# Optimization experiments

Hardware: AMD Instinct MI355X
Metric: run time of the kernel (lower is better)

## Reference

```python
import jax, jax.numpy as jnp
import numpy as np
from jax import lax

# QuantumDMRGLayer (isolated_labelnode=True) as a pure MPS chain contraction.
# Per sample: contract each site's (2,m[,m]) tensor with the 2-dim input vector
# over the physical leg, then multiply the resulting bond matrices along the
# chain, inserting the (m,m,nblabels) output tensor after site pos_label.

B, L, M, NBL = 2048, 196, 16, 10  # batch, dimvec, bond_len, nblabels


def setup_inputs() -> dict:
    key = jax.random.key(0)
    k_in, k_mid, k_l, k_r, k_out = jax.random.split(key, 5)
    # std chosen for numerical stability of a 196-long matrix product:
    # each site matrix is x0*A[0]+x1*A[1] with x~N(0,1), so effective per-site
    # gain ~ std*sqrt(2*m); std = 1/sqrt(2*m) keeps the product O(1).
    std = 1.0 / np.sqrt(2.0 * M)
    inputs = jax.random.normal(k_in, (B, L, 2), dtype=jnp.float32)
    eye2m = jnp.eye(M, dtype=jnp.float32)[:2, :]  # eye(max(2,m))[0:2,:] -> (2, m)
    A_left = eye2m + 1e-3 * jax.random.normal(k_l, (2, M), dtype=jnp.float32)
    A_right = eye2m + 1e-3 * jax.random.normal(k_r, (2, M), dtype=jnp.float32)
    A_mid = std * jax.random.normal(k_mid, (L - 2, 2, M, M), dtype=jnp.float32)
    T_out = (1.0 / np.sqrt(M)) * jax.random.normal(k_out, (M, M, NBL), dtype=jnp.float32)
    return {
        "inputs": inputs,
        "A_left": A_left,
        "A_mid": A_mid,
        "A_right": A_right,
        "T_out": T_out,
        "pos_label": 98,
    }


def reference(inputs, A_left, A_mid, A_right, T_out, pos_label):
    # Contract physical legs: interior site i (1..L-2) -> batched (m,m) matrix.
    mats = jnp.einsum("bsd,sdij->sbij", inputs[:, 1:-1, :], A_mid)  # (L-2, B, m, m)
    v_left = jnp.einsum("bd,dm->bm", inputs[:, 0, :], A_left)       # (B, m)
    v_right = jnp.einsum("bd,dm->bm", inputs[:, -1, :], A_right)    # (B, m)

    def step_l(v, Mx):  # v @ M, batched
        return jnp.einsum("bm,bmn->bn", v, Mx), None

    def step_r(v, Mx):  # M @ v, batched (sweep from the right end inward)
        return jnp.einsum("bmn,bn->bm", Mx, v), None

    # sites 1..pos_label feed the left bond of the output node,
    # sites pos_label+1..L-2 feed the right bond.
    left, _ = lax.scan(step_l, v_left, mats[:pos_label])
    right, _ = lax.scan(step_r, v_right, mats[pos_label:], reverse=True)
    return jnp.einsum("bm,mnl,bn->bl", left, T_out, right)  # (B, nblabels)
```

## Files before the change

### kernel.cpp

```cpp
#include <hip/hip_runtime.h>


typedef __attribute__((ext_vector_type(8))) short short8;
typedef __attribute__((ext_vector_type(16))) float floatx16;

#define GSITE_DW 512
#define GDIR_DW (100 * GSITE_DW)
#define STATE_DW (2 * GDIR_DW)

__device__ __forceinline__ unsigned bf16_rne(unsigned u) {
    return (u + 0x7FFFu + ((u >> 16) & 1u)) >> 16;
}

__global__ __launch_bounds__(256)
void prep_kernel(const float* __restrict__ AM, unsigned* __restrict__ WS)
{
    int t = blockIdx.x * 256 + threadIdx.x;
    const int w    = t & 3;  t >>= 2;
    const int lane = t & 63; t >>= 6;
    const int p    = t % 100;
    const int dir  = t / 100;
    const int kb = (lane >> 5) << 3;
    const int r  = lane & 31;
    const int rr = (r & 0x13) | ((r & 4) << 1) | ((r & 8) >> 1);
    const int d = rr >> 4, nn = rr & 15;
    const int lim = dir ? 96 : 98;
    const int a = dir ? (193 - p) : p;
    const int k0 = kb + 2 * w;
    float g0 = 0.f, g1 = 0.f;
    if (p < lim) {
        const float* Ab = AM + a * 512 + d * 256;
        if (dir == 0) { g0 = Ab[k0 * 16 + nn]; g1 = Ab[(k0 + 1) * 16 + nn]; }
        else          { g0 = Ab[nn * 16 + k0]; g1 = Ab[nn * 16 + k0 + 1]; }
    }
    const unsigned u0 = __float_as_uint(g0), u1 = __float_as_uint(g1);
    const unsigned h0 = bf16_rne(u0), h1 = bf16_rne(u1);
    const float l0f = g0 - __uint_as_float(h0 << 16);
    const float l1f = g1 - __uint_as_float(h1 << 16);
    const unsigned lo0 = bf16_rne(__float_as_uint(l0f));
    const unsigned lo1 = bf16_rne(__float_as_uint(l1f));
    unsigned* gp = WS + (dir * 100 + p) * GSITE_DW;
    gp[lane * 4 + w]       = (h1 << 16) | h0;
    gp[256 + lane * 4 + w] = (lo1 << 16) | lo0;
}

__global__ __launch_bounds__(64, 1)
void chain_kernel(const float* __restrict__ X,
                  const float* __restrict__ AL,
                  const float* __restrict__ AR,
                  const unsigned* __restrict__ WS,
                  float* __restrict__ WST)
{
    const int lane = threadIdx.x;
    const int dir  = blockIdx.x & 1;
    const int s    = (blockIdx.x >> 1) * 32 + (lane & 31);
    const int kb   = (lane >> 5) << 3;
    const float* Xs = X + s * 392;
    const unsigned* Gb = WS + dir * GDIR_DW + lane * 4;
    const int lim = dir ? 96 : 98;

    float w[8];
    int4 vh4, vl4;
    auto pack = [&]() {
#pragma unroll
        for (int q = 0; q < 4; ++q) {
            const unsigned u0 = __float_as_uint(w[2 * q]);
            const unsigned u1 = __float_as_uint(w[2 * q + 1]);
            const unsigned h0 = u0 & 0xFFFF0000u, h1 = u1 & 0xFFFF0000u;
            const float l0 = w[2 * q]     - __uint_as_float(h0);
            const float l1 = w[2 * q + 1] - __uint_as_float(h1);
            ((unsigned*)&vh4)[q] = h1 | (h0 >> 16);
            ((unsigned*)&vl4)[q] = (__float_as_uint(l1) & 0xFFFF0000u) |
                                   (__float_as_uint(l0) >> 16);
        }
    };

    const float* Ai = dir ? AR : AL;
    const float2 xi = *(const float2*)(Xs + (dir ? 390 : 0));
#pragma unroll
    for (int j = 0; j < 8; ++j)
        w[j] = xi.x * Ai[kb + j] + xi.y * Ai[16 + kb + j];
    pack();

    int4 GH[4], GL[4];
    float2 xr[4];
#pragma unroll
    for (int i = 0; i < 4; ++i) {
        GH[i] = *(const int4*)(Gb + i * GSITE_DW);
        GL[i] = *(const int4*)(Gb + i * GSITE_DW + 256);
        xr[i] = *(const float2*)(Xs + (dir ? (388 - 2 * i) : (2 + 2 * i)));
    }

    for (int c = 0; c < 25; ++c) {
#pragma unroll
        for (int j4 = 0; j4 < 4; ++j4) {
            const int p = 4 * c + j4;
            if (p < lim) {
                const short8 ah = *(short8*)&GH[j4];
                const short8 al = *(short8*)&GL[j4];
                const short8 bh = *(short8*)&vh4;
                const short8 bl = *(short8*)&vl4;
                floatx16 D = {};
                D = __builtin_amdgcn_mfma_f32_32x32x16_bf16(ah, bh, D, 0, 0, 0);
                D = __builtin_amdgcn_mfma_f32_32x32x16_bf16(ah, bl, D, 0, 0, 0);
                D = __builtin_amdgcn_mfma_f32_32x32x16_bf16(al, bh, D, 0, 0, 0);
                const float2 xs = xr[j4];
#pragma unroll
                for (int j = 0; j < 8; ++j)
                    w[j] = fmaf(xs.x, D[j], xs.y * D[j + 8]);
                pack();
            }
            const int pn = (p + 4 < 100) ? p + 4 : 99;
            GH[j4] = *(const int4*)(Gb + pn * GSITE_DW);
            GL[j4] = *(const int4*)(Gb + pn * GSITE_DW + 256);
            xr[j4] = *(const float2*)(Xs + (dir ? (388 - 2 * pn) : (2 + 2 * pn)));
        }
    }

    float* st = WST + (dir * 2048 + s) * 16 + kb;
    *(float4*)(st)     = make_float4(w[0], w[1], w[2], w[3]);
    *(float4*)(st + 4) = make_float4(w[4], w[5], w[6], w[7]);
}

__global__ __launch_bounds__(256)
void out_kernel(const float* __restrict__ T, const float* __restrict__ WST,
                float* __restrict__ OUT)
{
    __shared__ float sT[2560];
    const int tid = threadIdx.x;
    for (int k = tid; k < 640; k += 256)
        ((float4*)sT)[k] = ((const float4*)T)[k];
    __syncthreads();
    const int t = blockIdx.x * 256 + tid;
    const int s = t / 10, l = t - s * 10;
    const float* L = WST + s * 16;
    const float* R = WST + 2048 * 16 + s * 16;
    const float4 Ra = *(const float4*)(R);
    const float4 Rb = *(const float4*)(R + 4);
    const float4 Rc = *(const float4*)(R + 8);
    const float4 Rd = *(const float4*)(R + 12);
    float acc = 0.f;
#pragma unroll
    for (int m = 0; m < 16; ++m) {
        const float lm = L[m];
        const float* Tp = sT + m * 160 + l;
        acc = fmaf(lm * Ra.x, Tp[0],   acc);
        acc = fmaf(lm * Ra.y, Tp[10],  acc);
        acc = fmaf(lm * Ra.z, Tp[20],  acc);
        acc = fmaf(lm * Ra.w, Tp[30],  acc);
        acc = fmaf(lm * Rb.x, Tp[40],  acc);
        acc = fmaf(lm * Rb.y, Tp[50],  acc);
        acc = fmaf(lm * Rb.z, Tp[60],  acc);
        acc = fmaf(lm * Rb.w, Tp[70],  acc);
        acc = fmaf(lm * Rc.x, Tp[80],  acc);
        acc = fmaf(lm * Rc.y, Tp[90],  acc);
        acc = fmaf(lm * Rc.z, Tp[100], acc);
        acc = fmaf(lm * Rc.w, Tp[110], acc);
        acc = fmaf(lm * Rd.x, Tp[120], acc);
        acc = fmaf(lm * Rd.y, Tp[130], acc);
        acc = fmaf(lm * Rd.z, Tp[140], acc);
        acc = fmaf(lm * Rd.w, Tp[150], acc);
    }
    OUT[t] = acc;
}

extern "C" void kernel_launch(void* const* d_in, const int* in_sizes, int n_in,
                              void* d_out, int out_size, void* d_ws, size_t ws_size,
                              hipStream_t stream)
{
    const float* X  = (const float*)d_in[0];
    const float* AL = (const float*)d_in[1];
    const float* AM = (const float*)d_in[2];
    const float* AR = (const float*)d_in[3];
    const float* T  = (const float*)d_in[4];
    (void)in_sizes; (void)n_in; (void)out_size; (void)ws_size;
    unsigned* WS = (unsigned*)d_ws;
    float* WST   = (float*)d_ws + STATE_DW;
    float* OUT   = (float*)d_out;

    hipLaunchKernelGGL(prep_kernel,  dim3(200), dim3(256), 0, stream, AM, WS);
    hipLaunchKernelGGL(chain_kernel, dim3(128), dim3(64),  0, stream,
                       X, AL, AR, WS, WST);
    hipLaunchKernelGGL(out_kernel,   dim3(80),  dim3(256), 0, stream,
                       T, WST, OUT);
}
```

Before: 86.87 us.

## Split MPS chain into parallel segment matrix products, combine in output kernel

Replaces the serial 98/96-step vector-matrix chain per sample with 8 independent segments of about 24 sites each. Each segment computes a full 16x16 product matrix by starting from the identity, and the segments run as 8192 wavefronts instead of 128. The combine kernel applies the boundary vectors and then the four segment matrices per side, followed by the output-tensor contraction. This trades a much longer serial latency chain for more parallel work and extra memory traffic, since each segment writes a full matrix per sample.

```diff
diff --git a/kernel.cpp b/kernel.cpp
--- a/kernel.cpp
+++ b/kernel.cpp
@@ -6,7 +6,7 @@
 
 #define GSITE_DW 512
 #define GDIR_DW (100 * GSITE_DW)
-#define STATE_DW (2 * GDIR_DW)
+#define SEG_OFF_DW (2 * GDIR_DW)
 
 __device__ __forceinline__ unsigned bf16_rne(unsigned u) {
     return (u + 0x7FFFu + ((u >> 16) & 1u)) >> 16;
@@ -44,20 +44,27 @@
     gp[256 + lane * 4 + w] = (lo1 << 16) | lo0;
 }
 
-__global__ __launch_bounds__(64, 1)
-void chain_kernel(const float* __restrict__ X,
-                  const float* __restrict__ AL,
-                  const float* __restrict__ AR,
-                  const unsigned* __restrict__ WS,
-                  float* __restrict__ WST)
-{
-    const int lane = threadIdx.x;
-    const int dir  = blockIdx.x & 1;
-    const int s    = (blockIdx.x >> 1) * 32 + (lane & 31);
-    const int kb   = (lane >> 5) << 3;
+__global__ __launch_bounds__(256, 4)
+void seg_kernel(const float* __restrict__ X,
+                const unsigned* __restrict__ WS,
+                float* __restrict__ S)
+{
+    const int lane = threadIdx.x & 63;
+    const int gw   = blockIdx.x * 4 + (threadIdx.x >> 6);
+    const int seg  = gw >> 10;
+    const int pair = gw & 1023;
+    const int dir  = seg >> 2;
+    const int si   = seg & 3;
+    int p0, p1;
+    if (dir == 0) { p0 = (si < 2) ? 25 * si : 50 + 24 * (si - 2);
+                    p1 = p0 + ((si < 2) ? 25 : 24); }
+    else          { p0 = 24 * si; p1 = p0 + 24; }
+
+    const int m  = lane & 15;
+    const int s  = pair * 2 + ((lane >> 4) & 1);
+    const int kb = (lane >> 5) << 3;
     const float* Xs = X + s * 392;
     const unsigned* Gb = WS + dir * GDIR_DW + lane * 4;
-    const int lim = dir ? 96 : 98;
 
     float w[8];
     int4 vh4, vl4;
@@ -75,27 +82,26 @@
         }
     };
 
-    const float* Ai = dir ? AR : AL;
-    const float2 xi = *(const float2*)(Xs + (dir ? 390 : 0));
 #pragma unroll
     for (int j = 0; j < 8; ++j)
-        w[j] = xi.x * Ai[kb + j] + xi.y * Ai[16 + kb + j];
+        w[j] = (kb + j == m) ? 1.0f : 0.0f;
     pack();
 
     int4 GH[4], GL[4];
     float2 xr[4];
 #pragma unroll
     for (int i = 0; i < 4; ++i) {
-        GH[i] = *(const int4*)(Gb + i * GSITE_DW);
-        GL[i] = *(const int4*)(Gb + i * GSITE_DW + 256);
-        xr[i] = *(const float2*)(Xs + (dir ? (388 - 2 * i) : (2 + 2 * i)));
-    }
-
-    for (int c = 0; c < 25; ++c) {
+        const int p = p0 + i;
+        GH[i] = *(const int4*)(Gb + p * GSITE_DW);
+        GL[i] = *(const int4*)(Gb + p * GSITE_DW + 256);
+        xr[i] = *(const float2*)(Xs + (dir ? (388 - 2 * p) : (2 + 2 * p)));
+    }
+
+    for (int c = 0; c < 7; ++c) {
 #pragma unroll
         for (int j4 = 0; j4 < 4; ++j4) {
-            const int p = 4 * c + j4;
-            if (p < lim) {
+            const int p = p0 + 4 * c + j4;
+            if (p < p1) {
                 const short8 ah = *(short8*)&GH[j4];
                 const short8 al = *(short8*)&GL[j4];
                 const short8 bh = *(short8*)&vh4;
@@ -110,58 +116,107 @@
                     w[j] = fmaf(xs.x, D[j], xs.y * D[j + 8]);
                 pack();
             }
-            const int pn = (p + 4 < 100) ? p + 4 : 99;
+            int pn = p + 4;
+            if (pn >= p1) pn = 99;
             GH[j4] = *(const int4*)(Gb + pn * GSITE_DW);
             GL[j4] = *(const int4*)(Gb + pn * GSITE_DW + 256);
             xr[j4] = *(const float2*)(Xs + (dir ? (388 - 2 * pn) : (2 + 2 * pn)));
         }
     }
 
-    float* st = WST + (dir * 2048 + s) * 16 + kb;
-    *(float4*)(st)     = make_float4(w[0], w[1], w[2], w[3]);
-    *(float4*)(st + 4) = make_float4(w[4], w[5], w[6], w[7]);
+    float* Sp = S + ((seg * 2048 + s) << 8) + m;
+#pragma unroll
+    for (int j = 0; j < 8; ++j)
+        Sp[(kb + j) << 4] = w[j];
 }
 
 __global__ __launch_bounds__(256)
-void out_kernel(const float* __restrict__ T, const float* __restrict__ WST,
-                float* __restrict__ OUT)
+void comb_out_kernel(const float* __restrict__ X,
+                     const float* __restrict__ AL,
+                     const float* __restrict__ AR,
+                     const float* __restrict__ T,
+                     const float* __restrict__ S,
+                     float* __restrict__ OUT)
 {
     __shared__ float sT[2560];
+    __shared__ float sst[8][2][16];
     const int tid = threadIdx.x;
     for (int k = tid; k < 640; k += 256)
         ((float4*)sT)[k] = ((const float4*)T)[k];
+
+    const int sl    = tid >> 5;
+    const int chain = (tid >> 4) & 1;
+    const int n     = tid & 15;
+    const int s     = blockIdx.x * 8 + sl;
+    const float* Xs = X + s * 392;
+
+    float v;
+    if (chain == 0) {
+        const float2 x = *(const float2*)(Xs);
+        v = x.x * AL[n] + x.y * AL[16 + n];
+    } else {
+        const float2 x = *(const float2*)(Xs + 390);
+        v = x.x * AR[n] + x.y * AR[16 + n];
+    }
+
+#pragma unroll
+    for (int q = 0; q < 4; ++q) {
+        const int seg = chain * 4 + q;
+        const float4* Ps =
+            (const float4*)(S + ((seg * 2048 + s) << 8) + (n << 4));
+        const float4 a = Ps[0], b = Ps[1], c = Ps[2], d = Ps[3];
+        float t0 =      a.x * __shfl(v,  0, 16);
+        t0 = fmaf(a.y, __shfl(v,  1, 16), t0);
+        t0 = fmaf(a.z, __shfl(v,  2, 16), t0);
+        t0 = fmaf(a.w, __shfl(v,  3, 16), t0);
+        float t1 =      b.x * __shfl(v,  4, 16);
+        t1 = fmaf(b.y, __shfl(v,  5, 16), t1);
+        t1 = fmaf(b.z, __shfl(v,  6, 16), t1);
+        t1 = fmaf(b.w, __shfl(v,  7, 16), t1);
+        float t2 =      c.x * __shfl(v,  8, 16);
+        t2 = fmaf(c.y, __shfl(v,  9, 16), t2);
+        t2 = fmaf(c.z, __shfl(v, 10, 16), t2);
+        t2 = fmaf(c.w, __shfl(v, 11, 16), t2);
+        float t3 =      d.x * __shfl(v, 12, 16);
+        t3 = fmaf(d.y, __shfl(v, 13, 16), t3);
+        t3 = fmaf(d.z, __shfl(v, 14, 16), t3);
+        t3 = fmaf(d.w, __shfl(v, 15, 16), t3);
+        v = (t0 + t1) + (t2 + t3);
+    }
+    sst[sl][chain][n] = v;
     __syncthreads();
-    const int t = blockIdx.x * 256 + tid;
-    const int s = t / 10, l = t - s * 10;
-    const float* L = WST + s * 16;
-    const float* R = WST + 2048 * 16 + s * 16;
-    const float4 Ra = *(const float4*)(R);
-    const float4 Rb = *(const float4*)(R + 4);
-    const float4 Rc = *(const float4*)(R + 8);
-    const float4 Rd = *(const float4*)(R + 12);
-    float acc = 0.f;
-#pragma unroll
-    for (int m = 0; m < 16; ++m) {
-        const float lm = L[m];
-        const float* Tp = sT + m * 160 + l;
-        acc = fmaf(lm * Ra.x, Tp[0],   acc);
-        acc = fmaf(lm * Ra.y, Tp[10],  acc);
-        acc = fmaf(lm * Ra.z, Tp[20],  acc);
-        acc = fmaf(lm * Ra.w, Tp[30],  acc);
-        acc = fmaf(lm * Rb.x, Tp[40],  acc);
-        acc = fmaf(lm * Rb.y, Tp[50],  acc);
-        acc = fmaf(lm * Rb.z, Tp[60],  acc);
-        acc = fmaf(lm * Rb.w, Tp[70],  acc);
-        acc = fmaf(lm * Rc.x, Tp[80],  acc);
-        acc = fmaf(lm * Rc.y, Tp[90],  acc);
-        acc = fmaf(lm * Rc.z, Tp[100], acc);
-        acc = fmaf(lm * Rc.w, Tp[110], acc);
-        acc = fmaf(lm * Rd.x, Tp[120], acc);
-        acc = fmaf(lm * Rd.y, Tp[130], acc);
-        acc = fmaf(lm * Rd.z, Tp[140], acc);
-        acc = fmaf(lm * Rd.w, Tp[150], acc);
-    }
-    OUT[t] = acc;
+
+    if (tid < 80) {
+        const int s2 = tid / 10, l = tid - s2 * 10;
+        const float* L = sst[s2][0];
+        const float4 Ra = *(const float4*)&sst[s2][1][0];
+        const float4 Rb = *(const float4*)&sst[s2][1][4];
+        const float4 Rc = *(const float4*)&sst[s2][1][8];
+        const float4 Rd = *(const float4*)&sst[s2][1][12];
+        float acc = 0.f;
+#pragma unroll
+        for (int m = 0; m < 16; ++m) {
+            const float lm = L[m];
+            const float* Tp = sT + m * 160 + l;
+            acc = fmaf(lm * Ra.x, Tp[0],   acc);
+            acc = fmaf(lm * Ra.y, Tp[10],  acc);
+            acc = fmaf(lm * Ra.z, Tp[20],  acc);
+            acc = fmaf(lm * Ra.w, Tp[30],  acc);
+            acc = fmaf(lm * Rb.x, Tp[40],  acc);
+            acc = fmaf(lm * Rb.y, Tp[50],  acc);
+            acc = fmaf(lm * Rb.z, Tp[60],  acc);
+            acc = fmaf(lm * Rb.w, Tp[70],  acc);
+            acc = fmaf(lm * Rc.x, Tp[80],  acc);
+            acc = fmaf(lm * Rc.y, Tp[90],  acc);
+            acc = fmaf(lm * Rc.z, Tp[100], acc);
+            acc = fmaf(lm * Rc.w, Tp[110], acc);
+            acc = fmaf(lm * Rd.x, Tp[120], acc);
+            acc = fmaf(lm * Rd.y, Tp[130], acc);
+            acc = fmaf(lm * Rd.z, Tp[140], acc);
+            acc = fmaf(lm * Rd.w, Tp[150], acc);
+        }
+        OUT[(blockIdx.x * 8 + s2) * 10 + l] = acc;
+    }
 }
 
 extern "C" void kernel_launch(void* const* d_in, const int* in_sizes, int n_in,
@@ -175,12 +230,11 @@
     const float* T  = (const float*)d_in[4];
     (void)in_sizes; (void)n_in; (void)out_size; (void)ws_size;
     unsigned* WS = (unsigned*)d_ws;
-    float* WST   = (float*)d_ws + STATE_DW;
+    float* S     = (float*)d_ws + SEG_OFF_DW;
     float* OUT   = (float*)d_out;
 
-    hipLaunchKernelGGL(prep_kernel,  dim3(200), dim3(256), 0, stream, AM, WS);
-    hipLaunchKernelGGL(chain_kernel, dim3(128), dim3(64),  0, stream,
-                       X, AL, AR, WS, WST);
-    hipLaunchKernelGGL(out_kernel,   dim3(80),  dim3(256), 0, stream,
-                       T, WST, OUT);
-}
+    hipLaunchKernelGGL(prep_kernel,     dim3(200),  dim3(256), 0, stream, AM, WS);
+    hipLaunchKernelGGL(seg_kernel,      dim3(2048), dim3(256), 0, stream, X, WS, S);
+    hipLaunchKernelGGL(comb_out_kernel, dim3(256),  dim3(256), 0, stream,
+                       X, AL, AR, T, S, OUT);
+}
```

New measurement: 105.5 us. 1.21x slower.

## Split chain into parallel segments per wave and fuse output contraction

Applied to the files above, without the earlier changes.

Instead of one wave walking all ~98 sites per direction for 32 samples, each direction's chain is split into four segments handled by separate waves. Each wave propagates an identity matrix to form a 16x16 segment product for 4 samples, using two interleaved MFMA streams. The segment products are staged in shared memory, a small fp32 matvec sweep combines them with the boundary vectors, and the T_out contraction is fused into the same kernel, removing the out_kernel launch and the global state round-trip. This shortens the serial dependency chain and raises occupancy (512 blocks instead of 128 single-wave blocks), at the cost of extra MFMA work from computing full matrix products instead of vector products.

```diff
diff --git a/kernel.cpp b/kernel.cpp
--- a/kernel.cpp
+++ b/kernel.cpp
@@ -6,7 +6,6 @@
 
 #define GSITE_DW 512
 #define GDIR_DW (100 * GSITE_DW)
-#define STATE_DW (2 * GDIR_DW)
 
 __device__ __forceinline__ unsigned bf16_rne(unsigned u) {
     return (u + 0x7FFFu + ((u >> 16) & 1u)) >> 16;
@@ -44,124 +43,157 @@
     gp[256 + lane * 4 + w] = (lo1 << 16) | lo0;
 }
 
-__global__ __launch_bounds__(64, 1)
-void chain_kernel(const float* __restrict__ X,
+__global__ __launch_bounds__(512, 4)
+void fused_kernel(const float* __restrict__ X,
                   const float* __restrict__ AL,
                   const float* __restrict__ AR,
+                  const float* __restrict__ T,
                   const unsigned* __restrict__ WS,
-                  float* __restrict__ WST)
-{
-    const int lane = threadIdx.x;
-    const int dir  = blockIdx.x & 1;
-    const int s    = (blockIdx.x >> 1) * 32 + (lane & 31);
-    const int kb   = (lane >> 5) << 3;
-    const float* Xs = X + s * 392;
-    const unsigned* Gb = WS + dir * GDIR_DW + lane * 4;
-    const int lim = dir ? 96 : 98;
-
-    float w[8];
-    int4 vh4, vl4;
-    auto pack = [&]() {
-#pragma unroll
-        for (int q = 0; q < 4; ++q) {
-            const unsigned u0 = __float_as_uint(w[2 * q]);
-            const unsigned u1 = __float_as_uint(w[2 * q + 1]);
-            const unsigned h0 = u0 & 0xFFFF0000u, h1 = u1 & 0xFFFF0000u;
-            const float l0 = w[2 * q]     - __uint_as_float(h0);
-            const float l1 = w[2 * q + 1] - __uint_as_float(h1);
-            ((unsigned*)&vh4)[q] = h1 | (h0 >> 16);
-            ((unsigned*)&vl4)[q] = (__float_as_uint(l1) & 0xFFFF0000u) |
-                                   (__float_as_uint(l0) >> 16);
-        }
-    };
-
-    const float* Ai = dir ? AR : AL;
-    const float2 xi = *(const float2*)(Xs + (dir ? 390 : 0));
-#pragma unroll
-    for (int j = 0; j < 8; ++j)
-        w[j] = xi.x * Ai[kb + j] + xi.y * Ai[16 + kb + j];
-    pack();
-
-    int4 GH[4], GL[4];
-    float2 xr[4];
-#pragma unroll
-    for (int i = 0; i < 4; ++i) {
-        GH[i] = *(const int4*)(Gb + i * GSITE_DW);
-        GL[i] = *(const int4*)(Gb + i * GSITE_DW + 256);
-        xr[i] = *(const float2*)(Xs + (dir ? (388 - 2 * i) : (2 + 2 * i)));
-    }
-
-    for (int c = 0; c < 25; ++c) {
-#pragma unroll
-        for (int j4 = 0; j4 < 4; ++j4) {
-            const int p = 4 * c + j4;
-            if (p < lim) {
-                const short8 ah = *(short8*)&GH[j4];
-                const short8 al = *(short8*)&GL[j4];
-                const short8 bh = *(short8*)&vh4;
-                const short8 bl = *(short8*)&vl4;
-                floatx16 D = {};
-                D = __builtin_amdgcn_mfma_f32_32x32x16_bf16(ah, bh, D, 0, 0, 0);
-                D = __builtin_amdgcn_mfma_f32_32x32x16_bf16(ah, bl, D, 0, 0, 0);
-                D = __builtin_amdgcn_mfma_f32_32x32x16_bf16(al, bh, D, 0, 0, 0);
-                const float2 xs = xr[j4];
-#pragma unroll
-                for (int j = 0; j < 8; ++j)
-                    w[j] = fmaf(xs.x, D[j], xs.y * D[j + 8]);
-                pack();
-            }
-            const int pn = (p + 4 < 100) ? p + 4 : 99;
-            GH[j4] = *(const int4*)(Gb + pn * GSITE_DW);
-            GL[j4] = *(const int4*)(Gb + pn * GSITE_DW + 256);
-            xr[j4] = *(const float2*)(Xs + (dir ? (388 - 2 * pn) : (2 + 2 * pn)));
-        }
-    }
-
-    float* st = WST + (dir * 2048 + s) * 16 + kb;
-    *(float4*)(st)     = make_float4(w[0], w[1], w[2], w[3]);
-    *(float4*)(st + 4) = make_float4(w[4], w[5], w[6], w[7]);
-}
-
-__global__ __launch_bounds__(256)
-void out_kernel(const float* __restrict__ T, const float* __restrict__ WST,
-                float* __restrict__ OUT)
+                  float* __restrict__ OUT)
 {
     __shared__ float sT[2560];
-    const int tid = threadIdx.x;
-    for (int k = tid; k < 640; k += 256)
+    __shared__ float sS[8][4][16][17];
+    __shared__ float sv[4][2][16];
+
+    const int tid  = threadIdx.x;
+    const int lane = tid & 63;
+    const int wv   = tid >> 6;
+    for (int k = tid; k < 640; k += 512)
         ((float4*)sT)[k] = ((const float4*)T)[k];
+
+    const int dir = wv >> 2;
+    const int si  = wv & 3;
+    int p0, p1;
+    if (dir == 0) { p0 = (si < 2) ? 25 * si : 50 + 24 * (si - 2);
+                    p1 = p0 + ((si < 2) ? 25 : 24); }
+    else          { p0 = 24 * si; p1 = p0 + 24; }
+
+    const int sel = (lane >> 4) & 1;
+    const int m   = lane & 15;
+    const int kb  = (lane >> 5) << 3;
+    const int sb  = blockIdx.x * 4;
+    const float* Xs0 = X + (sb + sel) * 392;
+    const float* Xs1 = X + (sb + 2 + sel) * 392;
+    const unsigned* Gb = WS + dir * GDIR_DW + lane * 4;
+
+    float w0[8], w1[8];
+    int4 vh0, vl0, vh1, vl1;
+#pragma unroll
+    for (int j = 0; j < 8; ++j) w0[j] = (kb + j == m) ? 1.0f : 0.0f;
+#pragma unroll
+    for (int q = 0; q < 4; ++q) {
+        const unsigned h0 = __float_as_uint(w0[2 * q]) & 0xFFFF0000u;
+        const unsigned h1 = __float_as_uint(w0[2 * q + 1]) & 0xFFFF0000u;
+        ((unsigned*)&vh0)[q] = h1 | (h0 >> 16);
+        ((unsigned*)&vl0)[q] = 0;
+        w1[2 * q] = w0[2 * q]; w1[2 * q + 1] = w0[2 * q + 1];
+    }
+    vh1 = vh0; vl1 = vl0;
+
+    auto comb = [&](const floatx16& D, const float2 xs,
+                    float* wq, int4& vh, int4& vl) {
+#pragma unroll
+        for (int q = 0; q < 4; ++q) {
+            const float a0 = fmaf(xs.x, D[2 * q],     xs.y * D[2 * q + 8]);
+            const float a1 = fmaf(xs.x, D[2 * q + 1], xs.y * D[2 * q + 9]);
+            wq[2 * q] = a0; wq[2 * q + 1] = a1;
+            const unsigned u0 = __float_as_uint(a0);
+            const unsigned u1 = __float_as_uint(a1);
+            const float l0 = a0 - __uint_as_float(u0 & 0xFFFF0000u);
+            const float l1 = a1 - __uint_as_float(u1 & 0xFFFF0000u);
+            ((unsigned*)&vh)[q] = __builtin_amdgcn_perm(u1, u0, 0x07060302u);
+            ((unsigned*)&vl)[q] = __builtin_amdgcn_perm(
+                __float_as_uint(l1), __float_as_uint(l0), 0x07060302u);
+        }
+    };
+
+    int4 GH[2], GL[2];
+    float2 xr0[2], xr1[2];
+#pragma unroll
+    for (int i = 0; i < 2; ++i) {
+        const int p = p0 + i;
+        GH[i] = *(const int4*)(Gb + p * GSITE_DW);
+        GL[i] = *(const int4*)(Gb + p * GSITE_DW + 256);
+        const int xo = dir ? (388 - 2 * p) : (2 + 2 * p);
+        xr0[i] = *(const float2*)(Xs0 + xo);
+        xr1[i] = *(const float2*)(Xs1 + xo);
+    }
+
+    for (int c = 0; c < 14; ++c) {
+#pragma unroll
+        for (int j2 = 0; j2 < 2; ++j2) {
+            const int p = p0 + 2 * c + j2;
+            if (p < p1) {
+                const short8 ah  = *(const short8*)&GH[j2];
+                const short8 al  = *(const short8*)&GL[j2];
+                const short8 bh0 = *(const short8*)&vh0;
+                const short8 bl0 = *(const short8*)&vl0;
+                floatx16 D0 = {};
+                D0 = __builtin_amdgcn_mfma_f32_32x32x16_bf16(ah, bh0, D0, 0, 0, 0);
+                D0 = __builtin_amdgcn_mfma_f32_32x32x16_bf16(ah, bl0, D0, 0, 0, 0);
+                D0 = __builtin_amdgcn_mfma_f32_32x32x16_bf16(al, bh0, D0, 0, 0, 0);
+                comb(D0, xr0[j2], w0, vh0, vl0);
+                const short8 bh1 = *(const short8*)&vh1;
+                const short8 bl1 = *(const short8*)&vl1;
+                floatx16 D1 = {};
+                D1 = __builtin_amdgcn_mfma_f32_32x32x16_bf16(ah, bh1, D1, 0, 0, 0);
+                D1 = __builtin_amdgcn_mfma_f32_32x32x16_bf16(ah, bl1, D1, 0, 0, 0);
+                D1 = __builtin_amdgcn_mfma_f32_32x32x16_bf16(al, bh1, D1, 0, 0, 0);
+                comb(D1, xr1[j2], w1, vh1, vl1);
+            }
+            int pn = p + 2;
+            if (pn >= p1) pn = 99;
+            GH[j2] = *(const int4*)(Gb + pn * GSITE_DW);
+            GL[j2] = *(const int4*)(Gb + pn * GSITE_DW + 256);
+            const int xo = dir ? (388 - 2 * pn) : (2 + 2 * pn);
+            xr0[j2] = *(const float2*)(Xs0 + xo);
+            xr1[j2] = *(const float2*)(Xs1 + xo);
+        }
+    }
+
+#pragma unroll
+    for (int j = 0; j < 8; ++j) {
+        sS[wv][sel][kb + j][m]     = w0[j];
+        sS[wv][2 + sel][kb + j][m] = w1[j];
+    }
     __syncthreads();
-    const int t = blockIdx.x * 256 + tid;
-    const int s = t / 10, l = t - s * 10;
-    const float* L = WST + s * 16;
-    const float* R = WST + 2048 * 16 + s * 16;
-    const float4 Ra = *(const float4*)(R);
-    const float4 Rb = *(const float4*)(R + 4);
-    const float4 Rc = *(const float4*)(R + 8);
-    const float4 Rd = *(const float4*)(R + 12);
-    float acc = 0.f;
-#pragma unroll
-    for (int m = 0; m < 16; ++m) {
-        const float lm = L[m];
-        const float* Tp = sT + m * 160 + l;
-        acc = fmaf(lm * Ra.x, Tp[0],   acc);
-        acc = fmaf(lm * Ra.y, Tp[10],  acc);
-        acc = fmaf(lm * Ra.z, Tp[20],  acc);
-        acc = fmaf(lm * Ra.w, Tp[30],  acc);
-        acc = fmaf(lm * Rb.x, Tp[40],  acc);
-        acc = fmaf(lm * Rb.y, Tp[50],  acc);
-        acc = fmaf(lm * Rb.z, Tp[60],  acc);
-        acc = fmaf(lm * Rb.w, Tp[70],  acc);
-        acc = fmaf(lm * Rc.x, Tp[80],  acc);
-        acc = fmaf(lm * Rc.y, Tp[90],  acc);
-        acc = fmaf(lm * Rc.z, Tp[100], acc);
-        acc = fmaf(lm * Rc.w, Tp[110], acc);
-        acc = fmaf(lm * Rd.x, Tp[120], acc);
-        acc = fmaf(lm * Rd.y, Tp[130], acc);
-        acc = fmaf(lm * Rd.z, Tp[140], acc);
-        acc = fmaf(lm * Rd.w, Tp[150], acc);
-    }
-    OUT[t] = acc;
+
+    if (wv < 2) {
+        const int smp   = wv * 2 + (lane >> 5);
+        const int chain = (lane >> 4) & 1;
+        const int n     = lane & 15;
+        const float2 x  = *(const float2*)(X + (sb + smp) * 392 +
+                                           (chain ? 390 : 0));
+        const float* Ab = chain ? AR : AL;
+        float v = x.x * Ab[n] + x.y * Ab[16 + n];
+#pragma unroll
+        for (int q = 0; q < 4; ++q) {
+            const float* Srow = &sS[chain * 4 + q][smp][n][0];
+            float acc = 0.f;
+#pragma unroll
+            for (int mm = 0; mm < 16; ++mm)
+                acc = fmaf(Srow[mm], __shfl(v, mm, 16), acc);
+            v = acc;
+        }
+        sv[smp][chain][n] = v;
+
+        if (lane < 20) {
+            const int s2 = lane / 10, l = lane - s2 * 10;
+            const int sm = wv * 2 + s2;
+            const float* Lp = sv[sm][0];
+            const float* Rp = sv[sm][1];
+            float acc = 0.f;
+#pragma unroll
+            for (int mm = 0; mm < 16; ++mm) {
+                const float lm = Lp[mm];
+                const float* Tp = sT + mm * 160 + l;
+#pragma unroll
+                for (int nn = 0; nn < 16; ++nn)
+                    acc = fmaf(lm * Rp[nn], Tp[nn * 10], acc);
+            }
+            OUT[(sb + sm) * 10 + l] = acc;
+        }
+    }
 }
 
 extern "C" void kernel_launch(void* const* d_in, const int* in_sizes, int n_in,
@@ -175,12 +207,9 @@
     const float* T  = (const float*)d_in[4];
     (void)in_sizes; (void)n_in; (void)out_size; (void)ws_size;
     unsigned* WS = (unsigned*)d_ws;
-    float* WST   = (float*)d_ws + STATE_DW;
     float* OUT   = (float*)d_out;
 
     hipLaunchKernelGGL(prep_kernel,  dim3(200), dim3(256), 0, stream, AM, WS);
-    hipLaunchKernelGGL(chain_kernel, dim3(128), dim3(64),  0, stream,
-                       X, AL, AR, WS, WST);
-    hipLaunchKernelGGL(out_kernel,   dim3(80),  dim3(256), 0, stream,
-                       T, WST, OUT);
-}
+    hipLaunchKernelGGL(fused_kernel, dim3(512), dim3(512), 0, stream,
+                       X, AL, AR, T, WS, OUT);
+}
```

Result: slower. 94.40 us (+8.7%).

## Pre-multiply adjacent site tensors into pairs to halve serial chain steps

Applied to the files above, without the earlier changes.

The prep kernel now multiplies each pair of adjacent site tensors over the bond index for all four physical-index combinations, storing them as split hi/lo bf16 sets. The chain kernel then does one step per pair: six independent MFMAs whose outputs are combined with the four products of the two sites' input components. This halves the number of dependent MFMA-to-pack iterations on the serial critical path at the cost of more MFMAs per step and a heavier prep kernel with shared-memory matmuls.

```diff
diff --git a/kernel.cpp b/kernel.cpp
--- a/kernel.cpp
+++ b/kernel.cpp
@@ -4,44 +4,72 @@
 typedef __attribute__((ext_vector_type(8))) short short8;
 typedef __attribute__((ext_vector_type(16))) float floatx16;
 
-#define GSITE_DW 512
-#define GDIR_DW (100 * GSITE_DW)
-#define STATE_DW (2 * GDIR_DW)
+#define PSET_DW 512
+#define PAIR_DW (2 * PSET_DW)
+#define LSTEPS 49
+#define RSTEPS 48
+#define RBASE_DW (LSTEPS * PAIR_DW)
+#define WST_OFF_DW ((LSTEPS + RSTEPS) * PAIR_DW)
 
 __device__ __forceinline__ unsigned bf16_rne(unsigned u) {
     return (u + 0x7FFFu + ((u >> 16) & 1u)) >> 16;
 }
 
 __global__ __launch_bounds__(256)
-void prep_kernel(const float* __restrict__ AM, unsigned* __restrict__ WS)
-{
-    int t = blockIdx.x * 256 + threadIdx.x;
-    const int w    = t & 3;  t >>= 2;
-    const int lane = t & 63; t >>= 6;
-    const int p    = t % 100;
-    const int dir  = t / 100;
-    const int kb = (lane >> 5) << 3;
-    const int r  = lane & 31;
-    const int rr = (r & 0x13) | ((r & 4) << 1) | ((r & 8) >> 1);
-    const int d = rr >> 4, nn = rr & 15;
-    const int lim = dir ? 96 : 98;
-    const int a = dir ? (193 - p) : p;
-    const int k0 = kb + 2 * w;
-    float g0 = 0.f, g1 = 0.f;
-    if (p < lim) {
-        const float* Ab = AM + a * 512 + d * 256;
-        if (dir == 0) { g0 = Ab[k0 * 16 + nn]; g1 = Ab[(k0 + 1) * 16 + nn]; }
-        else          { g0 = Ab[nn * 16 + k0]; g1 = Ab[nn * 16 + k0 + 1]; }
-    }
-    const unsigned u0 = __float_as_uint(g0), u1 = __float_as_uint(g1);
-    const unsigned h0 = bf16_rne(u0), h1 = bf16_rne(u1);
-    const float l0f = g0 - __uint_as_float(h0 << 16);
-    const float l1f = g1 - __uint_as_float(h1 << 16);
-    const unsigned lo0 = bf16_rne(__float_as_uint(l0f));
-    const unsigned lo1 = bf16_rne(__float_as_uint(l1f));
-    unsigned* gp = WS + (dir * 100 + p) * GSITE_DW;
-    gp[lane * 4 + w]       = (h1 << 16) | h0;
-    gp[256 + lane * 4 + w] = (lo1 << 16) | lo0;
+void prep_pair(const float* __restrict__ AM, unsigned* __restrict__ WS)
+{
+    __shared__ float sA0[2][16][16];
+    __shared__ float sA1[2][16][16];
+    const int pidx = blockIdx.x;
+    const int tid  = threadIdx.x;
+    const int dir  = (pidx >= LSTEPS) ? 1 : 0;
+    const int t    = dir ? (pidx - LSTEPS) : pidx;
+    const int a0   = dir ? (192 - 2 * t) : (2 * t);
+    const int a1   = a0 + 1;
+
+    for (int i = tid; i < 512; i += 256) {
+        ((float*)sA0)[i] = AM[a0 * 512 + i];
+        ((float*)sA1)[i] = AM[a1 * 512 + i];
+    }
+    __syncthreads();
+
+    unsigned* gp = WS + (dir ? (RBASE_DW + t * PAIR_DW) : (t * PAIR_DW));
+    for (int u = tid; u < 512; u += 256) {
+        const int s_   = u >> 8;
+        const int lane = (u & 255) >> 2;
+        const int w_   = u & 3;
+        const int r    = lane & 31;
+        const int kb   = (lane >> 5) << 3;
+        const int d    = r >> 4;
+        const int rl   = r & 15;
+        const int sig  = (rl & 3) | ((rl & 4) << 1) | ((rl & 8) >> 1);
+        const int b0 = s_, b1 = d;
+        const int k0 = kb + 2 * w_;
+        float q0 = 0.f, q1 = 0.f;
+        if (dir == 0) {
+#pragma unroll
+            for (int m_ = 0; m_ < 16; ++m_) {
+                const float a1v = sA1[b1][m_][sig];
+                q0 = fmaf(sA0[b0][k0][m_],     a1v, q0);
+                q1 = fmaf(sA0[b0][k0 + 1][m_], a1v, q1);
+            }
+        } else {
+#pragma unroll
+            for (int m_ = 0; m_ < 16; ++m_) {
+                const float a0v = sA0[b0][sig][m_];
+                q0 = fmaf(a0v, sA1[b1][m_][k0],     q0);
+                q1 = fmaf(a0v, sA1[b1][m_][k0 + 1], q1);
+            }
+        }
+        const unsigned u0 = __float_as_uint(q0), u1 = __float_as_uint(q1);
+        const unsigned h0 = bf16_rne(u0), h1 = bf16_rne(u1);
+        const float l0f = q0 - __uint_as_float(h0 << 16);
+        const float l1f = q1 - __uint_as_float(h1 << 16);
+        const unsigned lo0 = bf16_rne(__float_as_uint(l0f));
+        const unsigned lo1 = bf16_rne(__float_as_uint(l1f));
+        gp[s_ * PSET_DW + lane * 4 + w_]       = (h1 << 16) | h0;
+        gp[s_ * PSET_DW + 256 + lane * 4 + w_] = (lo1 << 16) | lo0;
+    }
 }
 
 __global__ __launch_bounds__(64, 1)
@@ -56,8 +84,8 @@
     const int s    = (blockIdx.x >> 1) * 32 + (lane & 31);
     const int kb   = (lane >> 5) << 3;
     const float* Xs = X + s * 392;
-    const unsigned* Gb = WS + dir * GDIR_DW + lane * 4;
-    const int lim = dir ? 96 : 98;
+    const unsigned* Gb = WS + (dir ? RBASE_DW : 0) + lane * 4;
+    const int nsteps = dir ? RSTEPS : LSTEPS;
 
     float w[8];
     int4 vh4, vl4;
@@ -82,39 +110,52 @@
         w[j] = xi.x * Ai[kb + j] + xi.y * Ai[16 + kb + j];
     pack();
 
-    int4 GH[4], GL[4];
-    float2 xr[4];
-#pragma unroll
-    for (int i = 0; i < 4; ++i) {
-        GH[i] = *(const int4*)(Gb + i * GSITE_DW);
-        GL[i] = *(const int4*)(Gb + i * GSITE_DW + 256);
-        xr[i] = *(const float2*)(Xs + (dir ? (388 - 2 * i) : (2 + 2 * i)));
-    }
-
-    for (int c = 0; c < 25; ++c) {
-#pragma unroll
-        for (int j4 = 0; j4 < 4; ++j4) {
-            const int p = 4 * c + j4;
-            if (p < lim) {
-                const short8 ah = *(short8*)&GH[j4];
-                const short8 al = *(short8*)&GL[j4];
-                const short8 bh = *(short8*)&vh4;
-                const short8 bl = *(short8*)&vl4;
-                floatx16 D = {};
-                D = __builtin_amdgcn_mfma_f32_32x32x16_bf16(ah, bh, D, 0, 0, 0);
-                D = __builtin_amdgcn_mfma_f32_32x32x16_bf16(ah, bl, D, 0, 0, 0);
-                D = __builtin_amdgcn_mfma_f32_32x32x16_bf16(al, bh, D, 0, 0, 0);
-                const float2 xs = xr[j4];
-#pragma unroll
-                for (int j = 0; j < 8; ++j)
-                    w[j] = fmaf(xs.x, D[j], xs.y * D[j + 8]);
-                pack();
-            }
-            const int pn = (p + 4 < 100) ? p + 4 : 99;
-            GH[j4] = *(const int4*)(Gb + pn * GSITE_DW);
-            GL[j4] = *(const int4*)(Gb + pn * GSITE_DW + 256);
-            xr[j4] = *(const float2*)(Xs + (dir ? (388 - 2 * pn) : (2 + 2 * pn)));
+    int4 GH[2][2], GL[2][2];
+    float2 xp[2], xq[2];
+    auto ldstep = [&](int t, int slot) {
+        const unsigned* gp = Gb + t * PAIR_DW;
+        GH[slot][0] = *(const int4*)(gp);
+        GL[slot][0] = *(const int4*)(gp + 256);
+        GH[slot][1] = *(const int4*)(gp + PSET_DW);
+        GL[slot][1] = *(const int4*)(gp + PSET_DW + 256);
+        const int xo = dir ? (386 - 4 * t) : (4 * t + 2);
+        xp[slot] = *(const float2*)(Xs + xo);
+        xq[slot] = *(const float2*)(Xs + xo + 2);
+    };
+    ldstep(0, 0);
+    ldstep(1, 1);
+
+    for (int t = 0; t < nsteps; ++t) {
+        const int slot = t & 1;
+        const short8 ah0 = *(const short8*)&GH[slot][0];
+        const short8 al0 = *(const short8*)&GL[slot][0];
+        const short8 ah1 = *(const short8*)&GH[slot][1];
+        const short8 al1 = *(const short8*)&GL[slot][1];
+        const float2 xpc = xp[slot], xqc = xq[slot];
+        if (t + 2 < nsteps) ldstep(t + 2, slot);
+
+        const short8 bh = *(const short8*)&vh4;
+        const short8 bl = *(const short8*)&vl4;
+        floatx16 Dhh0 = {}, Dhl0 = {}, Dlh0 = {};
+        floatx16 Dhh1 = {}, Dhl1 = {}, Dlh1 = {};
+        Dhh0 = __builtin_amdgcn_mfma_f32_32x32x16_bf16(ah0, bh, Dhh0, 0, 0, 0);
+        Dhh1 = __builtin_amdgcn_mfma_f32_32x32x16_bf16(ah1, bh, Dhh1, 0, 0, 0);
+        Dhl0 = __builtin_amdgcn_mfma_f32_32x32x16_bf16(ah0, bl, Dhl0, 0, 0, 0);
+        Dhl1 = __builtin_amdgcn_mfma_f32_32x32x16_bf16(ah1, bl, Dhl1, 0, 0, 0);
+        Dlh0 = __builtin_amdgcn_mfma_f32_32x32x16_bf16(al0, bh, Dlh0, 0, 0, 0);
+        Dlh1 = __builtin_amdgcn_mfma_f32_32x32x16_bf16(al1, bh, Dlh1, 0, 0, 0);
+
+        const float c0 = xpc.x * xqc.x, c1 = xpc.x * xqc.y;
+        const float c2 = xpc.y * xqc.x, c3 = xpc.y * xqc.y;
+#pragma unroll
+        for (int j = 0; j < 8; ++j) {
+            const float e0  = (Dhh0[j]     + Dhl0[j])     + Dlh0[j];
+            const float e0h = (Dhh0[j + 8] + Dhl0[j + 8]) + Dlh0[j + 8];
+            const float e1  = (Dhh1[j]     + Dhl1[j])     + Dlh1[j];
+            const float e1h = (Dhh1[j + 8] + Dhl1[j + 8]) + Dlh1[j + 8];
+            w[j] = fmaf(c0, e0, fmaf(c1, e0h, fmaf(c2, e1, c3 * e1h)));
         }
+        pack();
     }
 
     float* st = WST + (dir * 2048 + s) * 16 + kb;
@@ -175,10 +216,10 @@
     const float* T  = (const float*)d_in[4];
     (void)in_sizes; (void)n_in; (void)out_size; (void)ws_size;
     unsigned* WS = (unsigned*)d_ws;
-    float* WST   = (float*)d_ws + STATE_DW;
+    float* WST   = (float*)d_ws + WST_OFF_DW;
     float* OUT   = (float*)d_out;
 
-    hipLaunchKernelGGL(prep_kernel,  dim3(200), dim3(256), 0, stream, AM, WS);
+    hipLaunchKernelGGL(prep_pair,    dim3(97),  dim3(256), 0, stream, AM, WS);
     hipLaunchKernelGGL(chain_kernel, dim3(128), dim3(64),  0, stream,
                        X, AL, AR, WS, WST);
     hipLaunchKernelGGL(out_kernel,   dim3(80),  dim3(256), 0, stream,
```

Result: slower. 124.9 us (+43.7%).
